# Performance work log

Measured on AMD Instinct MI355X. Metric: run time of the kernel, lower is better.

## Reference

```python
import jax, jax.numpy as jnp
import numpy as np

N_CHEM = 100000
N_PROT = 20000
D = 128           # hidden_channels, also input feature dim (lazy SAGEConv)
E = 600000        # edges chem->protein (reverse relation uses flipped index)
EL = 200000       # label edges for decoder
L = 3             # SAGEConv layers


def setup_inputs() -> dict:
    key = jax.random.key(0)
    ks = jax.random.split(key, 11)
    inp = {
        'x_chem':    jax.random.normal(ks[0], (N_CHEM, D), jnp.float32),
        'x_protein': jax.random.normal(ks[1], (N_PROT, D), jnp.float32),
        # Wl/bl/Wr stacked over [layer, relation]; relation 0 = chem->protein (dst protein),
        # relation 1 = protein->chem (dst chem). PyG SAGEConv: lin_l has bias, lin_r does not.
        'Wl': jax.random.normal(ks[2], (L, 2, D, D), jnp.float32) * 0.05,
        'bl': jax.random.normal(ks[3], (L, 2, D), jnp.float32) * 0.05,
        'Wr': jax.random.normal(ks[4], (L, 2, D, D), jnp.float32) * 0.05,
        'Wd': jax.random.normal(ks[5], (1, 2 * D), jnp.float32) * 0.05,
        'bd': jax.random.normal(ks[6], (1,), jnp.float32) * 0.05,
        'src_idx': jax.random.randint(ks[7], (E,), 0, N_CHEM, jnp.int64),
        'dst_idx': jax.random.randint(ks[8], (E,), 0, N_PROT, jnp.int64),
        'row': jax.random.randint(ks[9], (EL,), 0, N_CHEM, jnp.int64),
        'col': jax.random.randint(ks[10], (EL,), 0, N_PROT, jnp.int64),
    }
    return inp


def _sage(x_src, x_dst, s_idx, d_idx, Wl, bl, Wr, n_dst):
    # PyG SAGEConv (aggr='mean'): lin_l(mean_j x_src[j]) + lin_r(x_dst)
    msg = x_src[s_idx]                                   # [E, D] gather
    agg = jax.ops.segment_sum(msg, d_idx, num_segments=n_dst)
    deg = jax.ops.segment_sum(jnp.ones((s_idx.shape[0],), x_src.dtype), d_idx,
                              num_segments=n_dst)
    mean = agg / jnp.clip(deg, 1.0)[:, None]
    return mean @ Wl.T + bl + x_dst @ Wr.T


def reference(x_chem, x_protein, Wl, bl, Wr, Wd, bd, src_idx, dst_idx, row, col):
    h_c, h_p = x_chem, x_protein
    for l in range(L):
        new_p = _sage(h_c, h_p, src_idx, dst_idx, Wl[l, 0], bl[l, 0], Wr[l, 0], N_PROT)
        new_c = _sage(h_p, h_c, dst_idx, src_idx, Wl[l, 1], bl[l, 1], Wr[l, 1], N_CHEM)
        h_c, h_p = jax.nn.relu(new_c), jax.nn.relu(new_p)
    # EdgeDecoder: gather + concat + linear -> flat scores
    x = jnp.concatenate([h_c[row], h_p[col]], axis=-1)   # [EL, 2D]
    z = (x @ Wd.T + bd).reshape(-1)                      # [EL]
    return (z, x)
```

## Files before the change

### kernel.cpp

```cpp
#include <hip/hip_runtime.h>

#define D128 128

typedef __attribute__((ext_vector_type(8))) short bf16x8;
typedef __attribute__((ext_vector_type(4))) float f32x4;
typedef unsigned short u16;
typedef unsigned int u32;

__device__ __forceinline__ u16 f2b(float f) {
  union { float f; u32 u; } x; x.f = f;
  u32 r = x.u + 0x7fffu + ((x.u >> 16) & 1u);
  return (u16)(r >> 16);
}
__device__ __forceinline__ float b2f(short s) {
  union { u32 u; float f; } x; x.u = ((u32)(unsigned short)s) << 16; return x.f;
}

#define GLD16(gp, lp) __builtin_amdgcn_global_load_lds( \
    (const __attribute__((address_space(1))) void*)(gp), \
    (__attribute__((address_space(3))) void*)(lp), 16, 0, 0)

__global__ __launch_bounds__(256) void cvt_all_k(const float* __restrict__ xc, const float* __restrict__ xp,
                                                 const float* __restrict__ Wl, const float* __restrict__ Wr,
                                                 u16* __restrict__ B0, u16* __restrict__ Wcat,
                                                 int* __restrict__ zbase, int NP, int NT) {
  const int nqx = NT * 32;
  const int TOT = nqx + 49152 + (2 * NT) / 4;
  for (int i = blockIdx.x * 256 + threadIdx.x; i < TOT; i += gridDim.x * 256) {
    if (i < nqx) {
      const int r = i >> 5, c4 = (i & 31) << 2;
      const float* sp = (r < NP) ? &xp[(size_t)r * D128 + c4]
                                 : &xc[(size_t)(r - NP) * D128 + c4];
      float4 f = *(const float4*)sp;
      uint2 u;
      u.x = (u32)f2b(f.x) | ((u32)f2b(f.y) << 16);
      u.y = (u32)f2b(f.z) | ((u32)f2b(f.w) << 16);
      *(uint2*)&B0[(size_t)i * 4] = u;
    } else if (i < nqx + 49152) {
      const int t = (i - nqx) * 4;
      const int slice = t >> 15, j = (t >> 8) & 127, k = t & 255;
      const float* sw = (k < 128) ? &Wl[(size_t)slice * 16384 + j * 128 + k]
                                  : &Wr[(size_t)slice * 16384 + j * 128 + (k - 128)];
      float4 f = *(const float4*)sw;
      uint2 u;
      u.x = (u32)f2b(f.x) | ((u32)f2b(f.y) << 16);
      u.y = (u32)f2b(f.z) | ((u32)f2b(f.w) << 16);
      *(uint2*)&Wcat[t] = u;
    } else {
      const int z = i - nqx - 49152;
      int4 zv; zv.x = 0; zv.y = 0; zv.z = 0; zv.w = 0;
      ((int4*)zbase)[z] = zv;
    }
  }
}

__global__ __launch_bounds__(256) void degree_k(const int* __restrict__ src, const int* __restrict__ dst,
                                                int* deg, int NP, int E) {
  int e = blockIdx.x * 256 + threadIdx.x;
  if (e >= E) return;
  atomicAdd(&deg[dst[e]], 1);
  atomicAdd(&deg[NP + src[e]], 1);
}

__global__ __launch_bounds__(256) void scan_k(const int* __restrict__ deg, int* __restrict__ offp, int NT) {
  __shared__ int sh[256];
  const int c = blockIdx.x;
  const int tid = threadIdx.x;
  int pre = 0;
  const int lim = c * 2048;
  for (int i = tid; i < lim; i += 256) pre += deg[i];
  sh[tid] = pre; __syncthreads();
#pragma unroll
  for (int o = 128; o > 0; o >>= 1) {
    if (tid < o) sh[tid] += sh[tid + o];
    __syncthreads();
  }
  const int base_pre = sh[0];
  __syncthreads();
  const int base = lim + tid * 8;
  int v[8]; int s = 0;
#pragma unroll
  for (int u = 0; u < 8; ++u) { int i = base + u; v[u] = (i < NT) ? deg[i] : 0; s += v[u]; }
  sh[tid] = s; __syncthreads();
#pragma unroll
  for (int o = 1; o < 256; o <<= 1) {
    int t = (tid >= o) ? sh[tid - o] : 0;
    __syncthreads();
    sh[tid] += t;
    __syncthreads();
  }
  int run = sh[tid] - s + base_pre;
#pragma unroll
  for (int u = 0; u < 8; ++u) { int i = base + u; if (i < NT) offp[i] = run; run += v[u]; }
}

__global__ __launch_bounds__(256) void fill_k(const int* __restrict__ src, const int* __restrict__ dst,
                                              const int* __restrict__ offp, int* cur, int* adj,
                                              int NP, int E) {
  int e = blockIdx.x * 256 + threadIdx.x;
  if (e >= E) return;
  const int s = src[e], d = dst[e];
  const int cn = NP + s;
  int pp = atomicAdd(&cur[d], 1);  adj[offp[d] + pp] = cn;
  int pc = atomicAdd(&cur[cn], 1); adj[offp[cn] + pc] = d;
}

__global__ __launch_bounds__(256) void agg_k(const u16* __restrict__ hcur, u16* __restrict__ hnext,
                                             const int* __restrict__ adj, const int* __restrict__ offp,
                                             const int* __restrict__ deg, int NT) {
  const int v = blockIdx.x * 16 + (threadIdx.x >> 4);
  if (v >= NT) return;
  const int l16 = threadIdx.x & 15;
  const int s = offp[v], cnt = deg[v];
  float ac[8] = {0.f, 0.f, 0.f, 0.f, 0.f, 0.f, 0.f, 0.f};
  for (int n = 0; n < cnt; n += 16) {
    int batch = cnt - n; if (batch > 16) batch = 16;
    int idx = (l16 < batch) ? adj[s + n + l16] : 0;
    int j = 0;
    for (; j + 4 <= batch; j += 4) {
      const int i0 = __shfl(idx, j, 16);
      const int i1 = __shfl(idx, j + 1, 16);
      const int i2 = __shfl(idx, j + 2, 16);
      const int i3 = __shfl(idx, j + 3, 16);
      bf16x8 r0 = *(const bf16x8*)&hcur[(size_t)i0 * D128 + l16 * 8];
      bf16x8 r1 = *(const bf16x8*)&hcur[(size_t)i1 * D128 + l16 * 8];
      bf16x8 r2 = *(const bf16x8*)&hcur[(size_t)i2 * D128 + l16 * 8];
      bf16x8 r3 = *(const bf16x8*)&hcur[(size_t)i3 * D128 + l16 * 8];
#pragma unroll
      for (int k = 0; k < 8; ++k)
        ac[k] += (b2f(r0[k]) + b2f(r1[k])) + (b2f(r2[k]) + b2f(r3[k]));
    }
    for (; j < batch; ++j) {
      const int i0 = __shfl(idx, j, 16);
      bf16x8 r0 = *(const bf16x8*)&hcur[(size_t)i0 * D128 + l16 * 8];
#pragma unroll
      for (int k = 0; k < 8; ++k) ac[k] += b2f(r0[k]);
    }
  }
  const float inv = (cnt > 0) ? 1.f / (float)cnt : 0.f;
  uint4 pk;
  pk.x = (u32)f2b(ac[0] * inv) | ((u32)f2b(ac[1] * inv) << 16);
  pk.y = (u32)f2b(ac[2] * inv) | ((u32)f2b(ac[3] * inv) << 16);
  pk.z = (u32)f2b(ac[4] * inv) | ((u32)f2b(ac[5] * inv) << 16);
  pk.w = (u32)f2b(ac[6] * inv) | ((u32)f2b(ac[7] * inv) << 16);
  *(uint4*)&hnext[(size_t)v * D128 + l16 * 8] = pk;
}

__global__ __launch_bounds__(256) void gemm_both_k(u16* __restrict__ hnext, const u16* __restrict__ hcur,
                                                   const u16* __restrict__ Wcat_l, const float* __restrict__ bl_l,
                                                   int NP, int NT, int tilesP) {
  __shared__ u16 As[128 * 64];
  __shared__ u16 Bs[128 * 64];
  const int t = blockIdx.x;
  const bool isP = t < tilesP;
  const int rbase = isP ? t * 128 : NP + (t - tilesP) * 128;
  const int hi = isP ? NP : NT;
  const u16* __restrict__ W = Wcat_l + (isP ? 0 : 32768);
  const float* __restrict__ bias = bl_l + (isP ? 0 : 128);

  const int tid = threadIdx.x;
  const int w = tid >> 6, lane = tid & 63;
  const int wr = w >> 1, wc = w & 1;
  const int l15 = lane & 15, chi = lane >> 4;

  f32x4 acc[4][4];
#pragma unroll
  for (int m = 0; m < 4; ++m)
#pragma unroll
    for (int n = 0; n < 4; ++n) acc[m][n] = (f32x4){0.f, 0.f, 0.f, 0.f};

  for (int ks = 0; ks < 4; ++ks) {
    const int k0 = ks * 64;
    const u16* Xsrc = (k0 < 128) ? hnext : hcur;
    const int kb = k0 & 127;
    if (ks) __syncthreads();
#pragma unroll
    for (int q = 0; q < 4; ++q) {
      const int ibase = w * 256 + q * 64;
      const int i = ibase + lane;
      const int r = i >> 3;
      const int cg = (i & 7) ^ (r & 7);
      int rr = rbase + r; if (rr >= hi) rr = hi - 1;
      GLD16(Xsrc + (size_t)rr * D128 + kb + cg * 8, (char*)As + ibase * 16);
      GLD16(W + (size_t)r * 256 + k0 + cg * 8, (char*)Bs + ibase * 16);
    }
    __syncthreads();
#pragma unroll
    for (int kk = 0; kk < 2; ++kk) {
      bf16x8 a[4], bfr[4];
      const int c = kk * 4 + chi;
#pragma unroll
      for (int m = 0; m < 4; ++m) {
        const int r = wr * 64 + m * 16 + l15;
        a[m] = *(const bf16x8*)((const char*)As + (r * 8 + (c ^ (r & 7))) * 16);
      }
#pragma unroll
      for (int n = 0; n < 4; ++n) {
        const int j = wc * 64 + n * 16 + l15;
        bfr[n] = *(const bf16x8*)((const char*)Bs + (j * 8 + (c ^ (j & 7))) * 16);
      }
#pragma unroll
      for (int m = 0; m < 4; ++m)
#pragma unroll
        for (int n = 0; n < 4; ++n)
          acc[m][n] = __builtin_amdgcn_mfma_f32_16x16x32_bf16(a[m], bfr[n], acc[m][n], 0, 0, 0);
    }
  }
#pragma unroll
  for (int n = 0; n < 4; ++n) {
    const int col = wc * 64 + n * 16 + l15;
    const float bv = bias[col];
#pragma unroll
    for (int m = 0; m < 4; ++m) {
      const int rb2 = rbase + wr * 64 + m * 16 + chi * 4;
#pragma unroll
      for (int q = 0; q < 4; ++q) {
        const int row = rb2 + q;
        if (row < hi) {
          float vv = acc[m][n][q] + bv;
          vv = vv > 0.f ? vv : 0.f;
          hnext[(size_t)row * D128 + col] = f2b(vv);
        }
      }
    }
  }
}

__global__ __launch_bounds__(256) void decoder_k(const u16* __restrict__ hf,
                                                 const int* __restrict__ rowi, const int* __restrict__ coli,
                                                 const float* __restrict__ Wd, const float* __restrict__ bd,
                                                 float* __restrict__ out, int NP, int EL) {
  const int lane = threadIdx.x & 63;
  const int wid = blockIdx.x * 4 + (threadIdx.x >> 6);
  const int nw = gridDim.x * 4;
  const float4 wv = *(const float4*)&Wd[lane * 4];
  const float bdv = bd[0];
  for (int e = wid; e < EL; e += nw) {
    const int r = rowi[e], c = coli[e];
    const u16* hrow = (lane < 32) ? &hf[(size_t)(NP + r) * D128 + lane * 4]
                                  : &hf[(size_t)c * D128 + (lane * 4 - 128)];
    const ushort4 hb = *(const ushort4*)hrow;
    const float x0 = b2f((short)hb.x), x1 = b2f((short)hb.y);
    const float x2 = b2f((short)hb.z), x3 = b2f((short)hb.w);
    float p = x0 * wv.x + x1 * wv.y + x2 * wv.z + x3 * wv.w;
#pragma unroll
    for (int m = 1; m < 64; m <<= 1) p += __shfl_xor(p, m, 64);
    float4 st; st.x = x0; st.y = x1; st.z = x2; st.w = x3;
    *(float4*)&out[(size_t)EL + (size_t)e * 256 + lane * 4] = st;
    if (lane == 0) out[e] = p + bdv;
  }
}


extern "C" void kernel_launch(void* const* d_in, const int* in_sizes, int n_in,
                              void* d_out, int out_size, void* d_ws, size_t ws_size,
                              hipStream_t stream) {
  const float* x_chem = (const float*)d_in[0];
  const float* x_prot = (const float*)d_in[1];
  const float* Wl = (const float*)d_in[2];
  const float* bl = (const float*)d_in[3];
  const float* Wr = (const float*)d_in[4];
  const float* Wd = (const float*)d_in[5];
  const float* bd = (const float*)d_in[6];
  const int* src = (const int*)d_in[7];
  const int* dst = (const int*)d_in[8];
  const int* row = (const int*)d_in[9];
  const int* col = (const int*)d_in[10];

  int NC = in_sizes[0] / D128;
  int NP = in_sizes[1] / D128;
  int E  = in_sizes[7];
  int EL = in_sizes[9];
  int NT = NP + NC;
  int nchunk = (NT + 2047) / 2048;
  float* out = (float*)d_out;

  char* w = (char*)d_ws;
  size_t szT = (size_t)NT * D128 * 2;
  u16* B0 = (u16*)w; w += szT;
  u16* B1 = (u16*)w; w += szT;
  u16* B2 = (u16*)w; w += szT;
  u16* Wcat = (u16*)w; w += (size_t)6 * 128 * 256 * 2;
  int* deg  = (int*)w; w += (size_t)NT * 4;
  int* cur  = (int*)w; w += (size_t)NT * 4;
  int* offp = (int*)w; w += (size_t)NT * 4;
  int* adj  = (int*)w; w += (size_t)2 * E * 4;
  if ((size_t)(w - (char*)d_ws) > ws_size) return;

  cvt_all_k<<<2048, 256, 0, stream>>>(x_chem, x_prot, Wl, Wr, B0, Wcat, deg, NP, NT);

  int gE = (E + 255) / 256;
  degree_k<<<gE, 256, 0, stream>>>(src, dst, deg, NP, E);
  scan_k<<<nchunk, 256, 0, stream>>>(deg, offp, NT);
  fill_k<<<gE, 256, 0, stream>>>(src, dst, offp, cur, adj, NP, E);

  const int tilesP = (NP + 127) >> 7;
  const int tilesC = (NC + 127) >> 7;
  u16* bufs[4] = {B0, B1, B2, B1};
  for (int l = 0; l < 3; ++l) {
    const u16* hcur = bufs[l];
    u16* hnext = bufs[l + 1];
    agg_k<<<(NT + 15) / 16, 256, 0, stream>>>(hcur, hnext, adj, offp, deg, NT);
    gemm_both_k<<<tilesP + tilesC, 256, 0, stream>>>(hnext, hcur,
                                                     Wcat + (size_t)l * 65536,
                                                     bl + (size_t)l * 256,
                                                     NP, NT, tilesP);
  }

  decoder_k<<<2048, 256, 0, stream>>>(B1, row, col, Wd, bd, out, NP, EL);
}
```

Before: 483.5 us.

## Fuse degree counting into conversion kernel, prefetch adjacency, widen decoder loads

Folds the degree-count atomics into the fp32→bf16 conversion kernel and uses a memset to zero deg and cur, which removes one launch. The aggregation kernel now prefetches the next batch of neighbour indices and unrolls the gather by 8 to keep more loads in flight. The decoder handles two edges per wavefront with 16-byte loads and nontemporal stores for the large concatenated output. The risk is that atomics mixed into the streaming loop cause contention, and that the wider unroll raises register pressure.

```diff
diff --git a/kernel.cpp b/kernel.cpp
--- a/kernel.cpp
+++ b/kernel.cpp
@@ -20,12 +20,14 @@
     (const __attribute__((address_space(1))) void*)(gp), \
     (__attribute__((address_space(3))) void*)(lp), 16, 0, 0)
 
-__global__ __launch_bounds__(256) void cvt_all_k(const float* __restrict__ xc, const float* __restrict__ xp,
+__global__ __launch_bounds__(256) void cvt_deg_k(const float* __restrict__ xc, const float* __restrict__ xp,
                                                  const float* __restrict__ Wl, const float* __restrict__ Wr,
+                                                 const int* __restrict__ src, const int* __restrict__ dst,
                                                  u16* __restrict__ B0, u16* __restrict__ Wcat,
-                                                 int* __restrict__ zbase, int NP, int NT) {
+                                                 int* __restrict__ deg, int NP, int NT, int E) {
   const int nqx = NT * 32;
-  const int TOT = nqx + 49152 + (2 * NT) / 4;
+  const int ncvt = nqx + 49152;
+  const int TOT = ncvt + E;
   for (int i = blockIdx.x * 256 + threadIdx.x; i < TOT; i += gridDim.x * 256) {
     if (i < nqx) {
       const int r = i >> 5, c4 = (i & 31) << 2;
@@ -36,7 +38,7 @@
       u.x = (u32)f2b(f.x) | ((u32)f2b(f.y) << 16);
       u.y = (u32)f2b(f.z) | ((u32)f2b(f.w) << 16);
       *(uint2*)&B0[(size_t)i * 4] = u;
-    } else if (i < nqx + 49152) {
+    } else if (i < ncvt) {
       const int t = (i - nqx) * 4;
       const int slice = t >> 15, j = (t >> 8) & 127, k = t & 255;
       const float* sw = (k < 128) ? &Wl[(size_t)slice * 16384 + j * 128 + k]
@@ -47,19 +49,11 @@
       u.y = (u32)f2b(f.z) | ((u32)f2b(f.w) << 16);
       *(uint2*)&Wcat[t] = u;
     } else {
-      const int z = i - nqx - 49152;
-      int4 zv; zv.x = 0; zv.y = 0; zv.z = 0; zv.w = 0;
-      ((int4*)zbase)[z] = zv;
-    }
-  }
-}
-
-__global__ __launch_bounds__(256) void degree_k(const int* __restrict__ src, const int* __restrict__ dst,
-                                                int* deg, int NP, int E) {
-  int e = blockIdx.x * 256 + threadIdx.x;
-  if (e >= E) return;
-  atomicAdd(&deg[dst[e]], 1);
-  atomicAdd(&deg[NP + src[e]], 1);
+      const int e = i - ncvt;
+      atomicAdd(&deg[dst[e]], 1);
+      atomicAdd(&deg[NP + src[e]], 1);
+    }
+  }
 }
 
 __global__ __launch_bounds__(256) void scan_k(const int* __restrict__ deg, int* __restrict__ offp, int NT) {
@@ -113,29 +107,48 @@
   const int l16 = threadIdx.x & 15;
   const int s = offp[v], cnt = deg[v];
   float ac[8] = {0.f, 0.f, 0.f, 0.f, 0.f, 0.f, 0.f, 0.f};
+  int idx = (l16 < cnt) ? adj[s + l16] : 0;
   for (int n = 0; n < cnt; n += 16) {
-    int batch = cnt - n; if (batch > 16) batch = 16;
-    int idx = (l16 < batch) ? adj[s + n + l16] : 0;
+    const int batch = (cnt - n < 16) ? (cnt - n) : 16;
+    const int nrem = cnt - n - 16;
+    const int idxn = (nrem > 0 && l16 < nrem) ? adj[s + n + 16 + l16] : 0;
     int j = 0;
-    for (; j + 4 <= batch; j += 4) {
-      const int i0 = __shfl(idx, j, 16);
-      const int i1 = __shfl(idx, j + 1, 16);
-      const int i2 = __shfl(idx, j + 2, 16);
-      const int i3 = __shfl(idx, j + 3, 16);
+    for (; j + 8 <= batch; j += 8) {
+      int i0 = __shfl(idx, j, 16),     i1 = __shfl(idx, j + 1, 16);
+      int i2 = __shfl(idx, j + 2, 16), i3 = __shfl(idx, j + 3, 16);
+      int i4 = __shfl(idx, j + 4, 16), i5 = __shfl(idx, j + 5, 16);
+      int i6 = __shfl(idx, j + 6, 16), i7 = __shfl(idx, j + 7, 16);
       bf16x8 r0 = *(const bf16x8*)&hcur[(size_t)i0 * D128 + l16 * 8];
       bf16x8 r1 = *(const bf16x8*)&hcur[(size_t)i1 * D128 + l16 * 8];
       bf16x8 r2 = *(const bf16x8*)&hcur[(size_t)i2 * D128 + l16 * 8];
       bf16x8 r3 = *(const bf16x8*)&hcur[(size_t)i3 * D128 + l16 * 8];
+      bf16x8 r4 = *(const bf16x8*)&hcur[(size_t)i4 * D128 + l16 * 8];
+      bf16x8 r5 = *(const bf16x8*)&hcur[(size_t)i5 * D128 + l16 * 8];
+      bf16x8 r6 = *(const bf16x8*)&hcur[(size_t)i6 * D128 + l16 * 8];
+      bf16x8 r7 = *(const bf16x8*)&hcur[(size_t)i7 * D128 + l16 * 8];
+#pragma unroll
+      for (int k = 0; k < 8; ++k)
+        ac[k] += ((b2f(r0[k]) + b2f(r1[k])) + (b2f(r2[k]) + b2f(r3[k])))
+               + ((b2f(r4[k]) + b2f(r5[k])) + (b2f(r6[k]) + b2f(r7[k])));
+    }
+    for (; j + 4 <= batch; j += 4) {
+      int i0 = __shfl(idx, j, 16),     i1 = __shfl(idx, j + 1, 16);
+      int i2 = __shfl(idx, j + 2, 16), i3 = __shfl(idx, j + 3, 16);
+      bf16x8 r0 = *(const bf16x8*)&hcur[(size_t)i0 * D128 + l16 * 8];
+      bf16x8 r1 = *(const bf16x8*)&hcur[(size_t)i1 * D128 + l16 * 8];
+      bf16x8 r2 = *(const bf16x8*)&hcur[(size_t)i2 * D128 + l16 * 8];
+      bf16x8 r3 = *(const bf16x8*)&hcur[(size_t)i3 * D128 + l16 * 8];
 #pragma unroll
       for (int k = 0; k < 8; ++k)
         ac[k] += (b2f(r0[k]) + b2f(r1[k])) + (b2f(r2[k]) + b2f(r3[k]));
     }
     for (; j < batch; ++j) {
-      const int i0 = __shfl(idx, j, 16);
+      int i0 = __shfl(idx, j, 16);
       bf16x8 r0 = *(const bf16x8*)&hcur[(size_t)i0 * D128 + l16 * 8];
 #pragma unroll
       for (int k = 0; k < 8; ++k) ac[k] += b2f(r0[k]);
     }
+    idx = idxn;
   }
   const float inv = (cnt > 0) ? 1.f / (float)cnt : 0.f;
   uint4 pk;
@@ -230,24 +243,35 @@
                                                  const int* __restrict__ rowi, const int* __restrict__ coli,
                                                  const float* __restrict__ Wd, const float* __restrict__ bd,
                                                  float* __restrict__ out, int NP, int EL) {
+  typedef __attribute__((ext_vector_type(8))) unsigned short u16x8;
   const int lane = threadIdx.x & 63;
+  const int half = lane >> 5;
+  const int l32 = lane & 31;
   const int wid = blockIdx.x * 4 + (threadIdx.x >> 6);
   const int nw = gridDim.x * 4;
-  const float4 wv = *(const float4*)&Wd[lane * 4];
+  float wvv[8];
+#pragma unroll
+  for (int k = 0; k < 8; ++k) wvv[k] = Wd[l32 * 8 + k];
   const float bdv = bd[0];
-  for (int e = wid; e < EL; e += nw) {
+  for (int e = wid * 2 + half; e < EL; e += nw * 2) {
     const int r = rowi[e], c = coli[e];
-    const u16* hrow = (lane < 32) ? &hf[(size_t)(NP + r) * D128 + lane * 4]
-                                  : &hf[(size_t)c * D128 + (lane * 4 - 128)];
-    const ushort4 hb = *(const ushort4*)hrow;
-    const float x0 = b2f((short)hb.x), x1 = b2f((short)hb.y);
-    const float x2 = b2f((short)hb.z), x3 = b2f((short)hb.w);
-    float p = x0 * wv.x + x1 * wv.y + x2 * wv.z + x3 * wv.w;
-#pragma unroll
-    for (int m = 1; m < 64; m <<= 1) p += __shfl_xor(p, m, 64);
-    float4 st; st.x = x0; st.y = x1; st.z = x2; st.w = x3;
-    *(float4*)&out[(size_t)EL + (size_t)e * 256 + lane * 4] = st;
-    if (lane == 0) out[e] = p + bdv;
+    const size_t hrow = (l32 < 16) ? ((size_t)(NP + r) * D128 + l32 * 8)
+                                   : ((size_t)c * D128 + (l32 - 16) * 8);
+    const u16x8 hb = *(const u16x8*)&hf[hrow];
+    float x0 = b2f((short)hb[0]), x1 = b2f((short)hb[1]);
+    float x2 = b2f((short)hb[2]), x3 = b2f((short)hb[3]);
+    float x4 = b2f((short)hb[4]), x5 = b2f((short)hb[5]);
+    float x6 = b2f((short)hb[6]), x7 = b2f((short)hb[7]);
+    float p = x0 * wvv[0] + x1 * wvv[1] + x2 * wvv[2] + x3 * wvv[3]
+            + x4 * wvv[4] + x5 * wvv[5] + x6 * wvv[6] + x7 * wvv[7];
+#pragma unroll
+    for (int m = 1; m < 32; m <<= 1) p += __shfl_xor(p, m, 64);
+    float* xo = out + (size_t)EL + (size_t)e * 256 + l32 * 8;
+    f32x4 lo = {x0, x1, x2, x3};
+    f32x4 hi2 = {x4, x5, x6, x7};
+    __builtin_nontemporal_store(lo, (f32x4*)xo);
+    __builtin_nontemporal_store(hi2, (f32x4*)(xo + 4));
+    if (l32 == 0) __builtin_nontemporal_store(p + bdv, &out[e]);
   }
 }
 
@@ -287,12 +311,12 @@
   int* adj  = (int*)w; w += (size_t)2 * E * 4;
   if ((size_t)(w - (char*)d_ws) > ws_size) return;
 
-  cvt_all_k<<<2048, 256, 0, stream>>>(x_chem, x_prot, Wl, Wr, B0, Wcat, deg, NP, NT);
-
-  int gE = (E + 255) / 256;
-  degree_k<<<gE, 256, 0, stream>>>(src, dst, deg, NP, E);
+  (void)hipMemsetAsync(deg, 0, (size_t)2 * NT * 4, stream);
+
+  cvt_deg_k<<<2048, 256, 0, stream>>>(x_chem, x_prot, Wl, Wr, src, dst,
+                                      B0, Wcat, deg, NP, NT, E);
   scan_k<<<nchunk, 256, 0, stream>>>(deg, offp, NT);
-  fill_k<<<gE, 256, 0, stream>>>(src, dst, offp, cur, adj, NP, E);
+  fill_k<<<(E + 255) / 256, 256, 0, stream>>>(src, dst, offp, cur, adj, NP, E);
 
   const int tilesP = (NP + 127) >> 7;
   const int tilesC = (NC + 127) >> 7;
```

After: 492.2 us. About the same (+1.8%).
